# Optimization experiments

Hardware: AMD Instinct MI355X
Metric: run time of the kernel (lower is better)

Reference implementation:

```python
import jax, jax.numpy as jnp
import numpy as np

EPS = 1e-8  # torch.cosine_similarity default eps


def setup_inputs() -> dict:
    key = jax.random.key(0)
    ks = jax.random.split(key, 6)
    B, U, P, H = 256, 128, 64, 768
    utt_output = jax.random.normal(ks[0], (U, B, H), dtype=jnp.float32)
    pheno_output = jax.random.normal(ks[1], (P, B, H), dtype=jnp.float32)
    # Conv1d(in=U, out=U, kernel=P) weight: [out, in, kernel]
    w_utt = jax.random.normal(ks[2], (U, U, P), dtype=jnp.float32) / np.sqrt(U * P)
    b_utt = jax.random.normal(ks[3], (U,), dtype=jnp.float32) * 0.01
    # Conv1d(in=P, out=P, kernel=U) weight: [out, in, kernel]
    w_pheno = jax.random.normal(ks[4], (P, P, U), dtype=jnp.float32) / np.sqrt(P * U)
    b_pheno = jax.random.normal(ks[5], (P,), dtype=jnp.float32) * 0.01
    return {"utt_output": utt_output, "pheno_output": pheno_output,
            "w_utt": w_utt, "b_utt": b_utt, "w_pheno": w_pheno, "b_pheno": b_pheno}


def reference(utt_output, pheno_output, w_utt, b_utt, w_pheno, b_pheno):
    # [len, B, H] -> [B, len, H]
    u = jnp.swapaxes(utt_output, 0, 1)    # [B, U, H]
    p = jnp.swapaxes(pheno_output, 0, 1)  # [B, P, H]
    # cosine similarity matrix c[b,i,j] = <u_i, p_j> / (max(|u_i|,eps)*max(|p_j|,eps))
    un = u / jnp.maximum(jnp.linalg.norm(u, axis=-1, keepdims=True), EPS)
    pn = p / jnp.maximum(jnp.linalg.norm(p, axis=-1, keepdims=True), EPS)
    c = jnp.einsum('buh,bph->bup', un, pn)  # [B, U, P]
    # Conv1d with kernel covering the full width -> output length 1, i.e. an einsum
    row_logits = jnp.einsum('bup,oup->bo', c, w_utt) + b_utt        # [B, U]
    col_logits = jnp.einsum('bup,opu->bo', c, w_pheno) + b_pheno    # [B, P]
    row_attention = jax.nn.softmax(row_logits, axis=-1)
    col_attention = jax.nn.softmax(col_logits, axis=-1)
    return row_attention, col_attention
```

## Files before the change

### kernel.cpp

```cpp
#include <hip/hip_runtime.h>
#include <stdint.h>

#define Bn 256
#define Un 128
#define Pn 64
#define Hn 768
#define Ototal 192
#define KC 16

#define LDU 40
#define LDB 72

typedef short s4v __attribute__((ext_vector_type(4)));
typedef short s8v __attribute__((ext_vector_type(8)));
typedef float f4v __attribute__((ext_vector_type(4)));

__device__ __forceinline__ short f2bf(float x) {
  union { float f; uint32_t u; } c; c.f = x;
  uint32_t r = (c.u + 0x7fffu + ((c.u >> 16) & 1u)) >> 16;
  return (short)(r & 0xffffu);
}

__device__ __forceinline__ float dot4(float4 v) {
  return v.x * v.x + v.y * v.y + v.z * v.z + v.w * v.w;
}

__global__ void __launch_bounds__(512) phaseAW(const float* __restrict__ utt,
                                               const float* __restrict__ ph,
                                               ushort* __restrict__ Cbf,
                                               const float* __restrict__ w_utt,
                                               const float* __restrict__ w_ph,
                                               ushort* __restrict__ Wbf) {
  __shared__ __align__(16) float smemf[64 * 129];
  char* smem = (char*)smemf;
  const int bx = blockIdx.x;
  const int t = threadIdx.x;

  if (bx >= 512) {
    if (bx < 2560) {
      int idx = (bx - 512) * 512 + t;
      Wbf[idx] = (ushort)f2bf(w_utt[idx]);
      return;
    }
    float* tile = smemf;
    const int oc = bx - 2560;
    const float* src = w_ph + (size_t)oc * 8192;
#pragma unroll
    for (int itr = 0; itr < 4; ++itr) {
      int idx = itr * 2048 + t * 4;
      int j = idx >> 7, i = idx & 127;
      float4 v = *(const float4*)(src + idx);
      tile[j * 129 + i + 0] = v.x;
      tile[j * 129 + i + 1] = v.y;
      tile[j * 129 + i + 2] = v.z;
      tile[j * 129 + i + 3] = v.w;
    }
    __syncthreads();
    const size_t obase = (size_t)(128 + oc) * 8192;
#pragma unroll
    for (int itr = 0; itr < 4; ++itr) {
      int k = itr * 2048 + t * 4;
      int i = k >> 6, j = k & 63;
      s4v o4 = { f2bf(tile[(j + 0) * 129 + i]),
                 f2bf(tile[(j + 1) * 129 + i]),
                 f2bf(tile[(j + 2) * 129 + i]),
                 f2bf(tile[(j + 3) * 129 + i]) };
      *(s4v*)&Wbf[obase + k] = o4;
    }
    return;
  }

  short (*uA)[64 * LDU] = (short (*)[64 * LDU])(smem);
  short (*pB)[64 * LDU] = (short (*)[64 * LDU])(smem + 10240);
  float* s_inu = (float*)(smem + 20480);
  float* s_inp = (float*)(smem + 20736);

  const int b = bx >> 1, half = bx & 1;
  const int w = t >> 6, l = t & 63;

  const int r  = t >> 3;
  const int cc = (t & 7) * 4;

  const size_t rstride = (size_t)Bn * Hn;
  const float* ubase = utt + (size_t)b * Hn + (size_t)(half * 64 + r) * rstride + cc;
  const float* pbase = ph  + (size_t)b * Hn + (size_t)r * rstride + cc;

  const int m  = l & 15;
  const int ko = (l >> 4) * 8;
  const int it = w & 3;
  const int jp = w >> 2;
  const int lw = r * LDU + (t & 7) * 4;
  const int fo = (it * 16 + m) * LDU + ko;
  const int go = (jp * 32 + m) * LDU + ko;

  f4v zero4 = {0.f, 0.f, 0.f, 0.f};
  f4v acc0 = zero4, acc1 = zero4;
  float ssu = 0.f, ssp = 0.f;

  {
    float4 a  = *(const float4*)ubase;
    float4 p0 = *(const float4*)pbase;
    ssu += dot4(a); ssp += dot4(p0);
    s4v au = { f2bf(a.x),  f2bf(a.y),  f2bf(a.z),  f2bf(a.w)  };
    s4v pp = { f2bf(p0.x), f2bf(p0.y), f2bf(p0.z), f2bf(p0.w) };
    *(s4v*)&uA[0][lw] = au;
    *(s4v*)&pB[0][lw] = pp;
  }
  __syncthreads();

#pragma unroll 2
  for (int c = 0; c < 24; ++c) {
    const int cur = c & 1;
    float4 nu, np;
    if (c < 23) {
      nu = *(const float4*)(ubase + (c + 1) * 32);
      np = *(const float4*)(pbase + (c + 1) * 32);
    }
    s8v af  = *(const s8v*)&uA[cur][fo];
    s8v bf0 = *(const s8v*)&pB[cur][go];
    s8v bf1 = *(const s8v*)&pB[cur][go + 16 * LDU];
    acc0 = __builtin_amdgcn_mfma_f32_16x16x32_bf16(af, bf0, acc0, 0, 0, 0);
    acc1 = __builtin_amdgcn_mfma_f32_16x16x32_bf16(af, bf1, acc1, 0, 0, 0);
    if (c < 23) {
      ssu += dot4(nu); ssp += dot4(np);
      s4v au = { f2bf(nu.x), f2bf(nu.y), f2bf(nu.z), f2bf(nu.w) };
      s4v pp = { f2bf(np.x), f2bf(np.y), f2bf(np.z), f2bf(np.w) };
      *(s4v*)&uA[cur ^ 1][lw] = au;
      *(s4v*)&pB[cur ^ 1][lw] = pp;
    }
    __syncthreads();
  }

  ssu += __shfl_xor(ssu, 4); ssu += __shfl_xor(ssu, 2); ssu += __shfl_xor(ssu, 1);
  ssp += __shfl_xor(ssp, 4); ssp += __shfl_xor(ssp, 2); ssp += __shfl_xor(ssp, 1);
  if ((t & 7) == 0) {
    s_inu[r] = 1.f / fmaxf(sqrtf(ssu), 1e-8f);
    s_inp[r] = 1.f / fmaxf(sqrtf(ssp), 1e-8f);
  }
  __syncthreads();

  const int cl = l & 15;
  const int rq = (l >> 4) * 4;
#pragma unroll
  for (int jt = 0; jt < 2; ++jt) {
    int j = jp * 32 + jt * 16 + cl;
    float sj = s_inp[j];
    f4v a = (jt == 0) ? acc0 : acc1;
#pragma unroll
    for (int rr = 0; rr < 4; ++rr) {
      int il = it * 16 + rq + rr;
      float v = a[rr] * s_inu[il] * sj;
      Cbf[((size_t)b * Un + half * 64 + il) * Pn + j] = (ushort)f2bf(v);
    }
  }
}

__global__ void __launch_bounds__(256) phaseB(const ushort* __restrict__ Cbf,
                                              const ushort* __restrict__ Wbf,
                                              float* __restrict__ partial) {
  const int kc = blockIdx.x;
  const int mt = blockIdx.y;
  const int nt = blockIdx.z;
  const int t = threadIdx.x;
  const int w = t >> 6, l = t & 63;

  __shared__ short Ab[64 * LDB];
  __shared__ short Bb[64 * LDB];

  const int row = t >> 2;
  const int k16 = (t & 3) * 16;

  f4v zero4 = {0.f, 0.f, 0.f, 0.f};
  f4v acc[4] = {zero4, zero4, zero4, zero4};

  const ushort* Ag = Cbf + (size_t)(mt * 64 + row) * 8192 + kc * 512 + k16;
  const ushort* Bg = Wbf + (size_t)(nt * 64 + row) * 8192 + kc * 512 + k16;
  const int m  = l & 15;
  const int ko = (l >> 4) * 8;

  for (int c = 0; c < 8; ++c) {
    s8v av0 = *(const s8v*)(Ag + c * 64);
    s8v av1 = *(const s8v*)(Ag + c * 64 + 8);
    s8v bv0 = *(const s8v*)(Bg + c * 64);
    s8v bv1 = *(const s8v*)(Bg + c * 64 + 8);
    __syncthreads();
    *(s8v*)&Ab[row * LDB + k16]     = av0;
    *(s8v*)&Ab[row * LDB + k16 + 8] = av1;
    *(s8v*)&Bb[row * LDB + k16]     = bv0;
    *(s8v*)&Bb[row * LDB + k16 + 8] = bv1;
    __syncthreads();
#pragma unroll
    for (int ks = 0; ks < 2; ++ks) {
      s8v af = *(const s8v*)&Ab[(16 * w + m) * LDB + ks * 32 + ko];
#pragma unroll
      for (int jt = 0; jt < 4; ++jt) {
        s8v bf = *(const s8v*)&Bb[(16 * jt + m) * LDB + ks * 32 + ko];
        acc[jt] = __builtin_amdgcn_mfma_f32_16x16x32_bf16(af, bf, acc[jt], 0, 0, 0);
      }
    }
  }

  const int rq = (l >> 4) * 4;
#pragma unroll
  for (int jt = 0; jt < 4; ++jt) {
    int og = nt * 64 + 16 * jt + (l & 15);
#pragma unroll
    for (int r = 0; r < 4; ++r) {
      int bg = mt * 64 + 16 * w + rq + r;
      partial[((size_t)kc * Bn + bg) * Ototal + og] = acc[jt][r];
    }
  }
}

__global__ void __launch_bounds__(192) phaseC(const float* __restrict__ partial,
                                              const float* __restrict__ b_utt,
                                              const float* __restrict__ b_ph,
                                              float* __restrict__ out) {
  const int b = blockIdx.x;
  const int t = threadIdx.x;
  const int w = t >> 6, l = t & 63;

  float v = 0.f;
#pragma unroll
  for (int kc = 0; kc < KC; ++kc)
    v += partial[((size_t)kc * Bn + b) * Ototal + t];
  v += (t < Un) ? b_utt[t] : b_ph[t - Un];

  __shared__ float red[3];
  float mx = v;
  for (int o = 32; o >= 1; o >>= 1) mx = fmaxf(mx, __shfl_xor(mx, o));
  if (l == 0) red[w] = mx;
  __syncthreads();
  float gmax = (t < Un) ? fmaxf(red[0], red[1]) : red[2];
  float e = expf(v - gmax);
  float s = e;
  for (int o = 32; o >= 1; o >>= 1) s += __shfl_xor(s, o);
  __syncthreads();
  if (l == 0) red[w] = s;
  __syncthreads();
  float gs = (t < Un) ? (red[0] + red[1]) : red[2];
  float r = e / gs;
  if (t < Un) out[(size_t)b * Un + t] = r;
  else        out[(size_t)Bn * Un + (size_t)b * Pn + (t - Un)] = r;
}

extern "C" void kernel_launch(void* const* d_in, const int* in_sizes, int n_in,
                              void* d_out, int out_size, void* d_ws, size_t ws_size,
                              hipStream_t stream) {
  const float* utt   = (const float*)d_in[0];
  const float* ph    = (const float*)d_in[1];
  const float* w_utt = (const float*)d_in[2];
  const float* b_utt = (const float*)d_in[3];
  const float* w_ph  = (const float*)d_in[4];
  const float* b_ph  = (const float*)d_in[5];

  char* ws = (char*)d_ws;
  ushort* Cbf     = (ushort*)(ws);
  ushort* Wbf     = (ushort*)(ws + 4194304);
  float*  partial = (float*)(ws + 7340032);

  phaseAW<<<dim3(2624), dim3(512), 0, stream>>>(utt, ph, Cbf, w_utt, w_ph, Wbf);
  phaseB <<<dim3(KC, 4, 3), dim3(256), 0, stream>>>(Cbf, Wbf, partial);
  phaseC <<<dim3(Bn), dim3(192), 0, stream>>>(partial, b_utt, b_ph, (float*)d_out);
}
```

Measured before the change: 208.0 us.

## Deepen global prefetch to four stages and remap blocks for batch locality

The cosine-similarity phase now holds four stages of global float4 loads in registers instead of one, so memory latency is hidden further ahead of the MFMA work. It fully unrolls the 24-step loop and replaces __syncthreads with an explicit LDS-only waitcnt plus s_barrier, so outstanding global loads no longer stall each barrier. The block index is also remapped so that consecutive blocks cover neighbouring batch indices with both halves grouped together. This raises register use and relies on the manual barrier being correct.

```diff
diff --git a/kernel.cpp b/kernel.cpp
--- a/kernel.cpp
+++ b/kernel.cpp
@@ -75,7 +75,8 @@
   float* s_inu = (float*)(smem + 20480);
   float* s_inp = (float*)(smem + 20736);
 
-  const int b = bx >> 1, half = bx & 1;
+  const int b    = (bx & 7) | ((bx >> 4) << 3);
+  const int half = (bx >> 3) & 1;
   const int w = t >> 6, l = t & 63;
 
   const int r  = t >> 3;
@@ -97,38 +98,51 @@
   f4v acc0 = zero4, acc1 = zero4;
   float ssu = 0.f, ssp = 0.f;
 
+  float4 pu[4], pp[4];
+  pu[0] = *(const float4*)(ubase);
+  pp[0] = *(const float4*)(pbase);
+  pu[1] = *(const float4*)(ubase + 32);
+  pp[1] = *(const float4*)(pbase + 32);
+  pu[2] = *(const float4*)(ubase + 64);
+  pp[2] = *(const float4*)(pbase + 64);
+  pu[3] = *(const float4*)(ubase + 96);
+  pp[3] = *(const float4*)(pbase + 96);
+
   {
-    float4 a  = *(const float4*)ubase;
-    float4 p0 = *(const float4*)pbase;
-    ssu += dot4(a); ssp += dot4(p0);
-    s4v au = { f2bf(a.x),  f2bf(a.y),  f2bf(a.z),  f2bf(a.w)  };
-    s4v pp = { f2bf(p0.x), f2bf(p0.y), f2bf(p0.z), f2bf(p0.w) };
+    float4 a = pu[0], q = pp[0];
+    ssu += dot4(a); ssp += dot4(q);
+    s4v au = { f2bf(a.x), f2bf(a.y), f2bf(a.z), f2bf(a.w) };
+    s4v qq = { f2bf(q.x), f2bf(q.y), f2bf(q.z), f2bf(q.w) };
     *(s4v*)&uA[0][lw] = au;
-    *(s4v*)&pB[0][lw] = pp;
-  }
-  __syncthreads();
-
-#pragma unroll 2
+    *(s4v*)&pB[0][lw] = qq;
+  }
+  asm volatile("s_waitcnt lgkmcnt(0)" ::: "memory");
+  __builtin_amdgcn_s_barrier();
+  __builtin_amdgcn_sched_barrier(0);
+
+#pragma unroll
   for (int c = 0; c < 24; ++c) {
     const int cur = c & 1;
-    float4 nu, np;
-    if (c < 23) {
-      nu = *(const float4*)(ubase + (c + 1) * 32);
-      np = *(const float4*)(pbase + (c + 1) * 32);
+    if (c + 4 < 24) {
+      pu[(c + 4) & 3] = *(const float4*)(ubase + (c + 4) * 32);
+      pp[(c + 4) & 3] = *(const float4*)(pbase + (c + 4) * 32);
     }
     s8v af  = *(const s8v*)&uA[cur][fo];
     s8v bf0 = *(const s8v*)&pB[cur][go];
     s8v bf1 = *(const s8v*)&pB[cur][go + 16 * LDU];
     acc0 = __builtin_amdgcn_mfma_f32_16x16x32_bf16(af, bf0, acc0, 0, 0, 0);
     acc1 = __builtin_amdgcn_mfma_f32_16x16x32_bf16(af, bf1, acc1, 0, 0, 0);
-    if (c < 23) {
-      ssu += dot4(nu); ssp += dot4(np);
-      s4v au = { f2bf(nu.x), f2bf(nu.y), f2bf(nu.z), f2bf(nu.w) };
-      s4v pp = { f2bf(np.x), f2bf(np.y), f2bf(np.z), f2bf(np.w) };
+    if (c + 1 < 24) {
+      float4 a = pu[(c + 1) & 3], q = pp[(c + 1) & 3];
+      ssu += dot4(a); ssp += dot4(q);
+      s4v au = { f2bf(a.x), f2bf(a.y), f2bf(a.z), f2bf(a.w) };
+      s4v qq = { f2bf(q.x), f2bf(q.y), f2bf(q.z), f2bf(q.w) };
       *(s4v*)&uA[cur ^ 1][lw] = au;
-      *(s4v*)&pB[cur ^ 1][lw] = pp;
-    }
-    __syncthreads();
+      *(s4v*)&pB[cur ^ 1][lw] = qq;
+    }
+    asm volatile("s_waitcnt lgkmcnt(0)" ::: "memory");
+    __builtin_amdgcn_s_barrier();
+    __builtin_amdgcn_sched_barrier(0);
   }
 
   ssu += __shfl_xor(ssu, 4); ssu += __shfl_xor(ssu, 2); ssu += __shfl_xor(ssu, 1);
```

New measurement: 213.3 us. 2.5% more time.

## Stage cosine-sim tiles in 256-wide K chunks with fewer barriers

Applied to the files above, without the earlier changes.

Rewrites the phaseAW similarity GEMM so each thread loads 32 contiguous floats per row, and each block stages a 64x256 bf16 chunk in a single-buffered LDS tile. This replaces 24 small double-buffered steps with 3 large ones, cutting barrier count and raising memory-level parallelism per thread. It also remaps block indices to interleave batches and halves, and adds a launch-bounds occupancy hint. The cost is larger LDS use (about 68 KB) and more registers, which may limit occupancy, and load and compute overlap less within each chunk.

```diff
diff --git a/kernel.cpp b/kernel.cpp
--- a/kernel.cpp
+++ b/kernel.cpp
@@ -8,7 +8,7 @@
 #define Ototal 192
 #define KC 16
 
-#define LDU 40
+#define LDC 264
 #define LDB 72
 
 typedef short s4v __attribute__((ext_vector_type(4)));
@@ -25,14 +25,20 @@
   return v.x * v.x + v.y * v.y + v.z * v.z + v.w * v.w;
 }
 
-__global__ void __launch_bounds__(512) phaseAW(const float* __restrict__ utt,
-                                               const float* __restrict__ ph,
-                                               ushort* __restrict__ Cbf,
-                                               const float* __restrict__ w_utt,
-                                               const float* __restrict__ w_ph,
-                                               ushort* __restrict__ Wbf) {
-  __shared__ __align__(16) float smemf[64 * 129];
-  char* smem = (char*)smemf;
+__device__ __forceinline__ s8v pack8(float4 x, float4 y) {
+  s8v r;
+  r[0] = f2bf(x.x); r[1] = f2bf(x.y); r[2] = f2bf(x.z); r[3] = f2bf(x.w);
+  r[4] = f2bf(y.x); r[5] = f2bf(y.y); r[6] = f2bf(y.z); r[7] = f2bf(y.w);
+  return r;
+}
+
+__global__ void __launch_bounds__(512, 4) phaseAW(const float* __restrict__ utt,
+                                                  const float* __restrict__ ph,
+                                                  ushort* __restrict__ Cbf,
+                                                  const float* __restrict__ w_utt,
+                                                  const float* __restrict__ w_ph,
+                                                  ushort* __restrict__ Wbf) {
+  __shared__ __align__(16) char smem[68096];
   const int bx = blockIdx.x;
   const int t = threadIdx.x;
 
@@ -42,7 +48,7 @@
       Wbf[idx] = (ushort)f2bf(w_utt[idx]);
       return;
     }
-    float* tile = smemf;
+    float* tile = (float*)smem;
     const int oc = bx - 2560;
     const float* src = w_ph + (size_t)oc * 8192;
 #pragma unroll
@@ -70,66 +76,89 @@
     return;
   }
 
-  short (*uA)[64 * LDU] = (short (*)[64 * LDU])(smem);
-  short (*pB)[64 * LDU] = (short (*)[64 * LDU])(smem + 10240);
-  float* s_inu = (float*)(smem + 20480);
-  float* s_inp = (float*)(smem + 20736);
-
-  const int b = bx >> 1, half = bx & 1;
+  short* uA = (short*)smem;
+  short* pB = (short*)(smem + 33792);
+  float* s_inu = (float*)(smem + 67584);
+  float* s_inp = s_inu + 64;
+
+  const int b    = (bx & 7) | ((bx >> 4) << 3);
+  const int half = (bx >> 3) & 1;
   const int w = t >> 6, l = t & 63;
 
-  const int r  = t >> 3;
-  const int cc = (t & 7) * 4;
+  const int r = t >> 3;
+  const int q = t & 7;
 
   const size_t rstride = (size_t)Bn * Hn;
-  const float* ubase = utt + (size_t)b * Hn + (size_t)(half * 64 + r) * rstride + cc;
-  const float* pbase = ph  + (size_t)b * Hn + (size_t)r * rstride + cc;
+  const float* ubase = utt + (size_t)b * Hn + (size_t)(half * 64 + r) * rstride + q * 32;
+  const float* pbase = ph  + (size_t)b * Hn + (size_t)r * rstride + q * 32;
 
   const int m  = l & 15;
   const int ko = (l >> 4) * 8;
   const int it = w & 3;
   const int jp = w >> 2;
-  const int lw = r * LDU + (t & 7) * 4;
-  const int fo = (it * 16 + m) * LDU + ko;
-  const int go = (jp * 32 + m) * LDU + ko;
+  const short* ArdU = &uA[(it * 16 + m) * LDC + ko];
+  const short* BrdP = &pB[(jp * 32 + m) * LDC + ko];
+  short* uW = &uA[r * LDC + q * 32];
+  short* pW = &pB[r * LDC + q * 32];
 
   f4v zero4 = {0.f, 0.f, 0.f, 0.f};
   f4v acc0 = zero4, acc1 = zero4;
   float ssu = 0.f, ssp = 0.f;
-
-  {
-    float4 a  = *(const float4*)ubase;
-    float4 p0 = *(const float4*)pbase;
-    ssu += dot4(a); ssp += dot4(p0);
-    s4v au = { f2bf(a.x),  f2bf(a.y),  f2bf(a.z),  f2bf(a.w)  };
-    s4v pp = { f2bf(p0.x), f2bf(p0.y), f2bf(p0.z), f2bf(p0.w) };
-    *(s4v*)&uA[0][lw] = au;
-    *(s4v*)&pB[0][lw] = pp;
-  }
-  __syncthreads();
-
-#pragma unroll 2
-  for (int c = 0; c < 24; ++c) {
-    const int cur = c & 1;
-    float4 nu, np;
-    if (c < 23) {
-      nu = *(const float4*)(ubase + (c + 1) * 32);
-      np = *(const float4*)(pbase + (c + 1) * 32);
-    }
-    s8v af  = *(const s8v*)&uA[cur][fo];
-    s8v bf0 = *(const s8v*)&pB[cur][go];
-    s8v bf1 = *(const s8v*)&pB[cur][go + 16 * LDU];
-    acc0 = __builtin_amdgcn_mfma_f32_16x16x32_bf16(af, bf0, acc0, 0, 0, 0);
-    acc1 = __builtin_amdgcn_mfma_f32_16x16x32_bf16(af, bf1, acc1, 0, 0, 0);
-    if (c < 23) {
-      ssu += dot4(nu); ssp += dot4(np);
-      s4v au = { f2bf(nu.x), f2bf(nu.y), f2bf(nu.z), f2bf(nu.w) };
-      s4v pp = { f2bf(np.x), f2bf(np.y), f2bf(np.z), f2bf(np.w) };
-      *(s4v*)&uA[cur ^ 1][lw] = au;
-      *(s4v*)&pB[cur ^ 1][lw] = pp;
-    }
-    __syncthreads();
-  }
+  float4 u0, u1, u2, u3, u4, u5, u6, u7;
+  float4 p0, p1, p2, p3, p4, p5, p6, p7;
+
+#define LOADC(cc) do {                                                        \
+    const float* up_ = ubase + (cc) * 256;                                    \
+    const float* qp_ = pbase + (cc) * 256;                                    \
+    u0 = *(const float4*)(up_);      u1 = *(const float4*)(up_ + 4);          \
+    u2 = *(const float4*)(up_ + 8);  u3 = *(const float4*)(up_ + 12);         \
+    u4 = *(const float4*)(up_ + 16); u5 = *(const float4*)(up_ + 20);         \
+    u6 = *(const float4*)(up_ + 24); u7 = *(const float4*)(up_ + 28);         \
+    p0 = *(const float4*)(qp_);      p1 = *(const float4*)(qp_ + 4);          \
+    p2 = *(const float4*)(qp_ + 8);  p3 = *(const float4*)(qp_ + 12);         \
+    p4 = *(const float4*)(qp_ + 16); p5 = *(const float4*)(qp_ + 20);         \
+    p6 = *(const float4*)(qp_ + 24); p7 = *(const float4*)(qp_ + 28);         \
+  } while (0)
+
+#define STAGEC() do {                                                         \
+    ssu += dot4(u0) + dot4(u1) + dot4(u2) + dot4(u3)                          \
+         + dot4(u4) + dot4(u5) + dot4(u6) + dot4(u7);                         \
+    ssp += dot4(p0) + dot4(p1) + dot4(p2) + dot4(p3)                          \
+         + dot4(p4) + dot4(p5) + dot4(p6) + dot4(p7);                         \
+    *(s8v*)(uW)      = pack8(u0, u1); *(s8v*)(uW + 8)  = pack8(u2, u3);       \
+    *(s8v*)(uW + 16) = pack8(u4, u5); *(s8v*)(uW + 24) = pack8(u6, u7);       \
+    *(s8v*)(pW)      = pack8(p0, p1); *(s8v*)(pW + 8)  = pack8(p2, p3);       \
+    *(s8v*)(pW + 16) = pack8(p4, p5); *(s8v*)(pW + 24) = pack8(p6, p7);       \
+  } while (0)
+
+#define COMPC() do {                                                          \
+    _Pragma("unroll")                                                         \
+    for (int ks = 0; ks < 8; ++ks) {                                          \
+      s8v af  = *(const s8v*)(ArdU + ks * 32);                                \
+      s8v bf0 = *(const s8v*)(BrdP + ks * 32);                                \
+      s8v bf1 = *(const s8v*)(BrdP + 16 * LDC + ks * 32);                     \
+      acc0 = __builtin_amdgcn_mfma_f32_16x16x32_bf16(af, bf0, acc0, 0, 0, 0); \
+      acc1 = __builtin_amdgcn_mfma_f32_16x16x32_bf16(af, bf1, acc1, 0, 0, 0); \
+    }                                                                         \
+  } while (0)
+
+  LOADC(0); STAGEC();
+  __syncthreads();
+  LOADC(1);
+  COMPC();
+  __syncthreads();
+  STAGEC();
+  __syncthreads();
+  LOADC(2);
+  COMPC();
+  __syncthreads();
+  STAGEC();
+  __syncthreads();
+  COMPC();
+
+#undef LOADC
+#undef STAGEC
+#undef COMPC
 
   ssu += __shfl_xor(ssu, 4); ssu += __shfl_xor(ssu, 2); ssu += __shfl_xor(ssu, 1);
   ssp += __shfl_xor(ssp, 4); ssp += __shfl_xor(ssp, 2); ssp += __shfl_xor(ssp, 1);
```

Result: slower. 286.4 us (+37.6%).
